# Optimization experiments

Hardware: AMD Instinct MI355X
Metric: run time of the kernel (lower is better)

Reference implementation:

```python
import jax, jax.numpy as jnp
import numpy as np

HEADS = 8
DIM_HEAD = 64
DOWN = 2

def setup_inputs() -> dict:
    key = jax.random.key(0)
    ks = jax.random.split(key, 6)
    shp = (1, 128, 16, 32, 32)
    inner = HEADS * DIM_HEAD  # 512
    return {
        "x": jax.random.normal(ks[0], shp, dtype=jnp.float32),
        "context": jax.random.normal(ks[1], shp, dtype=jnp.float32),
        "Wq": jax.random.normal(ks[2], (inner, 128), dtype=jnp.float32) * 0.02,
        "Wk": jax.random.normal(ks[3], (inner, 128), dtype=jnp.float32) * 0.02,
        "Wv": jax.random.normal(ks[4], (inner, 128), dtype=jnp.float32) * 0.02,
        "Wo": jax.random.normal(ks[5], (128, inner), dtype=jnp.float32) * 0.02,
    }

def _avg_pool3d(c, f):
    b, ch, d, h, w = c.shape
    return c.reshape(b, ch, d // f, f, h // f, f, w // f, f).mean(axis=(3, 5, 7))

def reference(x, context, Wq, Wk, Wv, Wo):
    b, c, d1, h1, w1 = x.shape
    n = d1 * h1 * w1
    scale = DIM_HEAD ** -0.5
    xf = x.reshape(b, c, n)  # [b, c, N]
    # 1x1x1 conv == channel matmul
    q = jnp.einsum('oc,bcn->bon', Wq, xf).reshape(b, HEADS, DIM_HEAD, n)
    q = jnp.swapaxes(q, -2, -1)  # [b, h, N, dh]
    ctx = _avg_pool3d(context, DOWN)
    _, _, d2, h2, w2 = ctx.shape
    m = d2 * h2 * w2
    cf = ctx.reshape(b, c, m)
    k = jnp.einsum('oc,bcm->bom', Wk, cf).reshape(b, HEADS, DIM_HEAD, m)  # [b,h,dh,M]
    v = jnp.einsum('oc,bcm->bom', Wv, cf).reshape(b, HEADS, DIM_HEAD, m)
    v = jnp.swapaxes(v, -2, -1)  # [b, h, M, dh]
    scores = jnp.einsum('bhnd,bhdm->bhnm', q, k) * scale  # [b,h,N,M]
    attn = jax.nn.softmax(scores, axis=-1)
    out = jnp.einsum('bhnm,bhmd->bhnd', attn, v)  # [b,h,N,dh]
    out = jnp.swapaxes(out, -2, -1).reshape(b, HEADS * DIM_HEAD, n)  # [b,inner,N]
    y = jnp.einsum('oc,bcn->bon', Wo, out)
    return y.reshape(b, -1, d1, h1, w1)
```

## Files before the change

### kernel.cpp

```cpp
#include <hip/hip_runtime.h>

#define N_TOK 16384
#define M_TOK 2048
#define NHEADS 8
#define DH 64
#define CIN 128
#define INNER 512

typedef __attribute__((ext_vector_type(8))) short bf16x8;
typedef __attribute__((ext_vector_type(16))) float f32x16;
typedef __attribute__((ext_vector_type(4))) unsigned int u32x4;
typedef __attribute__((ext_vector_type(2))) unsigned int u32x2;

__device__ __forceinline__ unsigned short f2bf(float f) {
    unsigned u = __float_as_uint(f);
    u += 0x7fff + ((u >> 16) & 1);
    return (unsigned short)(u >> 16);
}

__device__ __forceinline__ unsigned cvtpk(float lo, float hi) {
    unsigned r;
    asm("v_cvt_pk_bf16_f32 %0, %1, %2" : "=v"(r) : "v"(lo), "v"(hi));
    return r;
}

__device__ __forceinline__ bf16x8 mk_bf16x8(unsigned a, unsigned b, unsigned c, unsigned d) {
    union { u32x4 w; bf16x8 h; } u;
    u.w = (u32x4){a, b, c, d};
    return u.h;
}

__device__ __forceinline__ void gload16(const void* g, void* l) {
    __builtin_amdgcn_global_load_lds(
        (const __attribute__((address_space(1))) unsigned int*)g,
        (__attribute__((address_space(3))) unsigned int*)l, 16, 0, 0);
}

__global__ __launch_bounds__(256) void prep_k(const float* __restrict__ Wq,
                                              const float* __restrict__ Wo,
                                              const float* __restrict__ cin,
                                              unsigned short* __restrict__ Wqb,
                                              unsigned short* __restrict__ Wob,
                                              float* __restrict__ cout) {
    if (blockIdx.x < 64) {
        int i = (blockIdx.x * 256 + threadIdx.x) * 8;
        const float* src; unsigned short* dst; float sc;
        if (i < 65536) { src = Wq + i; dst = Wqb + i; sc = 0.125f; }
        else           { src = Wo + (i - 65536); dst = Wob + (i - 65536); sc = 1.0f; }
        float4 a = *reinterpret_cast<const float4*>(src);
        float4 b = *reinterpret_cast<const float4*>(src + 4);
        unsigned short u[8] = { f2bf(a.x * sc), f2bf(a.y * sc), f2bf(a.z * sc), f2bf(a.w * sc),
                                f2bf(b.x * sc), f2bf(b.y * sc), f2bf(b.z * sc), f2bf(b.w * sc) };
        *reinterpret_cast<uint4*>(dst) = *reinterpret_cast<uint4*>(u);
    } else {
        int idx = (blockIdx.x - 64) * 256 + threadIdx.x;
        int c = idx >> 11, m = idx & 2047;
        int d2 = m >> 8, h2 = (m >> 4) & 15, w2 = m & 15;
        const float* b = cin + c * 16384 + d2 * 2048 + h2 * 64 + w2 * 2;
        float s = b[0] + b[1] + b[32] + b[33] + b[1024] + b[1025] + b[1056] + b[1057];
        cout[idx] = s * 0.125f;
    }
}

__global__ __launch_bounds__(256) void xT_k(const float* __restrict__ x,
                                            unsigned short* __restrict__ xb) {
    __shared__ unsigned short tile[64 * 132];
    const int t = threadIdx.x;
    const int n0 = blockIdx.x * 128;
    const int cb = blockIdx.y * 64;
#pragma unroll
    for (int cc2 = 0; cc2 < 2; ++cc2)
#pragma unroll
        for (int lp = 0; lp < 4; ++lp) {
            int id = lp * 256 + t;
            int row = id >> 5, ch = id & 31;
            float4 v = *reinterpret_cast<const float4*>(
                &x[(size_t)(cb + cc2 * 32 + row) * N_TOK + n0 + ch * 4]);
            unsigned short u[4] = { f2bf(v.x), f2bf(v.y), f2bf(v.z), f2bf(v.w) };
            *reinterpret_cast<uint2*>(&tile[(cc2 * 32 + row) * 132 + ch * 4]) =
                *reinterpret_cast<uint2*>(u);
        }
    __syncthreads();
#pragma unroll
    for (int lp = 0; lp < 4; ++lp) {
        int id = lp * 256 + t;
        int n = id >> 3, cg = id & 7;
        unsigned short u[8];
#pragma unroll
        for (int j = 0; j < 8; ++j) u[j] = tile[(cg * 8 + j) * 132 + n];
        *reinterpret_cast<uint4*>(&xb[(size_t)(n0 + n) * 128 + cb + cg * 8]) =
            *reinterpret_cast<uint4*>(u);
    }
}

__global__ __launch_bounds__(256) void kvproj_k(const float* __restrict__ ctx,
                                                const float* __restrict__ Wk,
                                                const float* __restrict__ Wv,
                                                unsigned short* __restrict__ Kb,
                                                unsigned short* __restrict__ Vb) {
    const int m0 = (blockIdx.x * 256 + threadIdx.x) * 2;
    const int o0 = blockIdx.y * 8;
    const float* W = blockIdx.z ? Wv : Wk;
    float acc[8][2];
#pragma unroll
    for (int j = 0; j < 8; ++j) { acc[j][0] = 0.f; acc[j][1] = 0.f; }
    for (int c4 = 0; c4 < CIN / 4; ++c4) {
        float xa[4][2];
#pragma unroll
        for (int cc = 0; cc < 4; ++cc)
            *reinterpret_cast<float2*>(xa[cc]) =
                *reinterpret_cast<const float2*>(&ctx[(size_t)(c4 * 4 + cc) * M_TOK + m0]);
#pragma unroll
        for (int j = 0; j < 8; ++j) {
            float4 wv = *reinterpret_cast<const float4*>(&W[(o0 + j) * CIN + c4 * 4]);
#pragma unroll
            for (int k = 0; k < 2; ++k) {
                acc[j][k] = fmaf(wv.x, xa[0][k], acc[j][k]);
                acc[j][k] = fmaf(wv.y, xa[1][k], acc[j][k]);
                acc[j][k] = fmaf(wv.z, xa[2][k], acc[j][k]);
                acc[j][k] = fmaf(wv.w, xa[3][k], acc[j][k]);
            }
        }
    }
    if (blockIdx.z) {
#pragma unroll
        for (int j = 0; j < 8; ++j) {
            unsigned w0 = (unsigned)f2bf(acc[j][0]) | ((unsigned)f2bf(acc[j][1]) << 16);
            *reinterpret_cast<unsigned*>(&Vb[(size_t)(o0 + j) * M_TOK + m0]) = w0;
        }
    } else {
        const int h = o0 >> 6, d0 = o0 & 63;
#pragma unroll
        for (int k = 0; k < 2; ++k) {
            unsigned short u[8];
#pragma unroll
            for (int j = 0; j < 8; ++j) u[j] = f2bf(acc[j][k]);
            *reinterpret_cast<uint4*>(&Kb[((size_t)h * M_TOK + m0 + k) * DH + d0]) =
                *reinterpret_cast<uint4*>(u);
        }
    }
}

__global__ __launch_bounds__(256) void qproj_k(const unsigned short* __restrict__ Wqb,
                                               const unsigned short* __restrict__ xb,
                                               unsigned short* __restrict__ Qb) {
    const int t = threadIdx.x;
    const int w = t >> 6, l = t & 63;
    const int la = l & 31, lg = l >> 5;
    const int n = blockIdx.x * 32 + la;

    bf16x8 bx[8];
#pragma unroll
    for (int ks = 0; ks < 8; ++ks)
        bx[ks] = *reinterpret_cast<const bf16x8*>(xb + (size_t)n * 128 + ks * 16 + lg * 8);

    f32x16 acc[4];
#pragma unroll
    for (int os = 0; os < 4; ++os) acc[os] = (f32x16){0,0,0,0,0,0,0,0,0,0,0,0,0,0,0,0};

#pragma unroll
    for (int os = 0; os < 4; ++os) {
        const int row = w * 128 + os * 32 + la;
#pragma unroll
        for (int ks = 0; ks < 8; ++ks) {
            bf16x8 aw = *reinterpret_cast<const bf16x8*>(Wqb + (size_t)row * 128 + ks * 16 + lg * 8);
            acc[os] = __builtin_amdgcn_mfma_f32_32x32x16_bf16(aw, bx[ks], acc[os], 0, 0, 0);
        }
    }
#pragma unroll
    for (int os = 0; os < 4; ++os) {
        const int h = w * 2 + (os >> 1);
        const int dbase = (os & 1) * 32 + 4 * lg;
#pragma unroll
        for (int rr = 0; rr < 4; ++rr) {
            unsigned p0 = cvtpk(acc[os][rr * 4 + 0], acc[os][rr * 4 + 1]);
            unsigned p1 = cvtpk(acc[os][rr * 4 + 2], acc[os][rr * 4 + 3]);
            uint2 pv = make_uint2(p0, p1);
            *reinterpret_cast<uint2*>(&Qb[((size_t)h * N_TOK + n) * DH + dbase + rr * 8]) = pv;
        }
    }
}

__global__ __launch_bounds__(256, 4) void attn_k(const unsigned short* __restrict__ Qb,
                                                 const unsigned short* __restrict__ Kb,
                                                 const unsigned short* __restrict__ Vb,
                                                 unsigned short* __restrict__ Ob) {
    __shared__ __align__(16) char smem[33792];
    __shared__ float rsinv[128];

    const int t = threadIdx.x;
    const int w = t >> 6, l = t & 63;
    const int la = l & 31, lg = l >> 5;
    const int bid = blockIdx.x;
    const int h = bid & 7;
    const int n0 = (bid >> 3) * 128;

    bf16x8 aq[4];
    {
        const unsigned short* qrow = Qb + ((size_t)h * N_TOK + n0 + w * 32 + la) * DH + lg * 8;
#pragma unroll
        for (int ks = 0; ks < 4; ++ks)
            aq[ks] = *reinterpret_cast<const bf16x8*>(qrow + ks * 16);
    }

    const int klane = (l >> 3) * 128 + (((l & 7) ^ (l >> 3)) << 4);
    const int vlane = (l >> 3) * 4096 + (((l & 7) ^ (l >> 3)) << 4);
    const char* gK = (const char*)Kb + (size_t)h * M_TOK * DH * 2 + w * 2048 + klane;
    const char* gV = (const char*)Vb + (size_t)h * DH * M_TOK * 2 + (size_t)w * 65536 + vlane;
    char* lKw = smem + w * 2048;

    auto stage = [&](int b, int tile) {
        char* lK = lKw + b * 16384;
        const char* sK = gK + (size_t)tile * 8192;
        const char* sV = gV + (size_t)tile * 128;
        gload16(sK, lK);
        gload16(sK + 1024, lK + 1024);
        gload16(sV, lK + 8192);
        gload16(sV + 32768, lK + 8192 + 1024);
    };

    f32x16 oacc0 = {0,0,0,0,0,0,0,0,0,0,0,0,0,0,0,0};
    f32x16 oacc1 = {0,0,0,0,0,0,0,0,0,0,0,0,0,0,0,0};
    float rs = 0.f;

    stage(0, 0);
    __syncthreads();

#pragma unroll 2
    for (int mt = 0; mt < M_TOK / 64; ++mt) {
        const int cb = (mt & 1) * 16384;
        if (mt < M_TOK / 64 - 1) stage((mt & 1) ^ 1, mt + 1);

#pragma unroll
        for (int ms = 0; ms < 2; ++ms) {
            f32x16 sacc = {0,0,0,0,0,0,0,0,0,0,0,0,0,0,0,0};
            __builtin_amdgcn_s_setprio(1);
#pragma unroll
            for (int ks = 0; ks < 4; ++ks) {
                const int row = ms * 32 + la;
                bf16x8 ak = *reinterpret_cast<const bf16x8*>(
                    smem + cb + row * 128 + ((32 * ks + 16 * lg) ^ ((row & 7) << 4)));
                sacc = __builtin_amdgcn_mfma_f32_32x32x16_bf16(ak, aq[ks], sacc, 0, 0, 0);
            }
            __builtin_amdgcn_s_setprio(0);
            float p[16];
#pragma unroll
            for (int r = 0; r < 16; ++r) { p[r] = __expf(sacc[r]); rs += p[r]; }
            u32x2 s0 = __builtin_amdgcn_permlane32_swap(cvtpk(p[0], p[1]),  cvtpk(p[4], p[5]),  false, false);
            u32x2 s1 = __builtin_amdgcn_permlane32_swap(cvtpk(p[2], p[3]),  cvtpk(p[6], p[7]),  false, false);
            u32x2 s2 = __builtin_amdgcn_permlane32_swap(cvtpk(p[8], p[9]),  cvtpk(p[12], p[13]), false, false);
            u32x2 s3 = __builtin_amdgcn_permlane32_swap(cvtpk(p[10], p[11]), cvtpk(p[14], p[15]), false, false);
            bf16x8 pa0 = mk_bf16x8(s0.x, s1.x, s0.y, s1.y);
            bf16x8 pa1 = mk_bf16x8(s2.x, s3.x, s2.y, s3.y);
            __builtin_amdgcn_s_setprio(1);
            {
                const int vrow = la, vs = (vrow & 7) << 4;
                bf16x8 bv0 = *reinterpret_cast<const bf16x8*>(
                    smem + cb + 8192 + vrow * 128 + ((64 * ms + 16 * lg) ^ vs));
                bf16x8 bv1 = *reinterpret_cast<const bf16x8*>(
                    smem + cb + 8192 + vrow * 128 + ((64 * ms + 32 + 16 * lg) ^ vs));
                oacc0 = __builtin_amdgcn_mfma_f32_32x32x16_bf16(pa0, bv0, oacc0, 0, 0, 0);
                oacc0 = __builtin_amdgcn_mfma_f32_32x32x16_bf16(pa1, bv1, oacc0, 0, 0, 0);
            }
            {
                const int vrow = 32 + la, vs = (vrow & 7) << 4;
                bf16x8 bv0 = *reinterpret_cast<const bf16x8*>(
                    smem + cb + 8192 + vrow * 128 + ((64 * ms + 16 * lg) ^ vs));
                bf16x8 bv1 = *reinterpret_cast<const bf16x8*>(
                    smem + cb + 8192 + vrow * 128 + ((64 * ms + 32 + 16 * lg) ^ vs));
                oacc1 = __builtin_amdgcn_mfma_f32_32x32x16_bf16(pa0, bv0, oacc1, 0, 0, 0);
                oacc1 = __builtin_amdgcn_mfma_f32_32x32x16_bf16(pa1, bv1, oacc1, 0, 0, 0);
            }
            __builtin_amdgcn_s_setprio(0);
        }
        __syncthreads();
    }

    rs += __shfl_xor(rs, 32);
    if (lg == 0) rsinv[w * 32 + la] = 1.0f / rs;

    __syncthreads();
    float* Ot = reinterpret_cast<float*>(smem);
#pragma unroll
    for (int dt = 0; dt < 2; ++dt)
#pragma unroll
        for (int r = 0; r < 16; r += 2) {
            int d = dt * 32 + la;
            int n = w * 32 + (r & 3) + 8 * (r >> 2) + 4 * lg;
            float2 v;
            v.x = dt ? oacc1[r] : oacc0[r];
            v.y = dt ? oacc1[r + 1] : oacc0[r + 1];
            *reinterpret_cast<float2*>(&Ot[d * 132 + n]) = v;
        }
    __syncthreads();
#pragma unroll
    for (int i = 0; i < 4; ++i) {
        int chunk = i * 256 + t;
        int n = chunk & 127, dg = chunk >> 7;
        float rv = rsinv[n];
        unsigned q[4];
#pragma unroll
        for (int jj = 0; jj < 4; ++jj) {
            float a = Ot[(dg * 8 + jj * 2) * 132 + n] * rv;
            float b = Ot[(dg * 8 + jj * 2 + 1) * 132 + n] * rv;
            q[jj] = cvtpk(a, b);
        }
        *reinterpret_cast<uint4*>(&Ob[(size_t)(n0 + n) * INNER + h * 64 + dg * 8]) =
            *reinterpret_cast<uint4*>(q);
    }
}

__global__ __launch_bounds__(256) void yproj_k(const unsigned short* __restrict__ Wob,
                                               const unsigned short* __restrict__ Ob,
                                               float* __restrict__ y) {
    const int t = threadIdx.x;
    const int w = t >> 6, l = t & 63;
    const int la = l & 31, lg = l >> 5;
    const int n = blockIdx.x * 32 + la;
    const int row = w * 32 + la;

    f32x16 acc = {0,0,0,0,0,0,0,0,0,0,0,0,0,0,0,0};
#pragma unroll 8
    for (int ks = 0; ks < 32; ++ks) {
        bf16x8 bo = *reinterpret_cast<const bf16x8*>(Ob + (size_t)n * INNER + ks * 16 + lg * 8);
        bf16x8 aw = *reinterpret_cast<const bf16x8*>(Wob + (size_t)row * INNER + ks * 16 + lg * 8);
        acc = __builtin_amdgcn_mfma_f32_32x32x16_bf16(aw, bo, acc, 0, 0, 0);
    }
#pragma unroll
    for (int rr = 0; rr < 4; ++rr)
#pragma unroll
        for (int q = 0; q < 4; ++q) {
            int o = w * 32 + 4 * lg + rr * 8 + q;
            y[(size_t)o * N_TOK + n] = acc[rr * 4 + q];
        }
}

extern "C" void kernel_launch(void* const* d_in, const int* in_sizes, int n_in,
                              void* d_out, int out_size, void* d_ws, size_t ws_size,
                              hipStream_t stream) {
    const float* x   = (const float*)d_in[0];
    const float* ctx = (const float*)d_in[1];
    const float* Wq  = (const float*)d_in[2];
    const float* Wk  = (const float*)d_in[3];
    const float* Wv  = (const float*)d_in[4];
    const float* Wo  = (const float*)d_in[5];
    float* y = (float*)d_out;

    char* W = (char*)d_ws;
    float* ctxp         = (float*)(W);
    unsigned short* Kb  = (unsigned short*)(W + 1u  * (1 << 20));
    unsigned short* Vb  = (unsigned short*)(W + 3u  * (1 << 20));
    unsigned short* xb  = (unsigned short*)(W + 5u  * (1 << 20));
    unsigned short* Wqb = (unsigned short*)(W + 9u  * (1 << 20));
    unsigned short* Wob = (unsigned short*)(W + 9u  * (1 << 20) + (256 << 10));
    unsigned short* Qb  = (unsigned short*)(W + 10u * (1 << 20));
    unsigned short* Ob  = (unsigned short*)(W + 26u * (1 << 20));

    prep_k<<<dim3(64 + (CIN * M_TOK) / 256), 256, 0, stream>>>(Wq, Wo, ctx, Wqb, Wob, ctxp);
    xT_k<<<dim3(N_TOK / 128, 2), 256, 0, stream>>>(x, xb);
    kvproj_k<<<dim3(M_TOK / 512, INNER / 8, 2), 256, 0, stream>>>(ctxp, Wk, Wv, Kb, Vb);
    qproj_k<<<dim3(N_TOK / 32), 256, 0, stream>>>(Wqb, xb, Qb);
    attn_k<<<dim3(N_TOK / 128 * NHEADS), 256, 0, stream>>>(Qb, Kb, Vb, Ob);
    yproj_k<<<dim3(N_TOK / 32), 256, 0, stream>>>(Wob, Ob, y);
}
```

Measured before the change: 145.3 us.

## Enlarge attention blocks to 512 threads sharing 128-token K/V tiles

Doubles the attention workgroup from 4 to 8 waves covering 256 query rows, so each K/V tile loaded into shared memory is reused by twice as many waves. The K/V tile per iteration grows from 64 to 128 context tokens, with a cooperative swizzled load across all threads and 64KB of double-buffered LDS. The output transpose epilogue is split into two passes to fit the existing staging layout. This lowers global K/V traffic and barrier count per unit of work, but the larger LDS footprint and block size may reduce occupancy, and the grid has half as many blocks.

```diff
diff --git a/kernel.cpp b/kernel.cpp
--- a/kernel.cpp
+++ b/kernel.cpp
@@ -181,19 +181,19 @@
     }
 }
 
-__global__ __launch_bounds__(256, 4) void attn_k(const unsigned short* __restrict__ Qb,
+__global__ __launch_bounds__(512, 4) void attn_k(const unsigned short* __restrict__ Qb,
                                                  const unsigned short* __restrict__ Kb,
                                                  const unsigned short* __restrict__ Vb,
                                                  unsigned short* __restrict__ Ob) {
-    __shared__ __align__(16) char smem[33792];
-    __shared__ float rsinv[128];
+    __shared__ __align__(16) char smem[65536];
+    __shared__ float rsinv[256];
 
     const int t = threadIdx.x;
     const int w = t >> 6, l = t & 63;
     const int la = l & 31, lg = l >> 5;
     const int bid = blockIdx.x;
     const int h = bid & 7;
-    const int n0 = (bid >> 3) * 128;
+    const int n0 = (bid >> 3) * 256;
 
     bf16x8 aq[4];
     {
@@ -203,20 +203,21 @@
             aq[ks] = *reinterpret_cast<const bf16x8*>(qrow + ks * 16);
     }
 
-    const int klane = (l >> 3) * 128 + (((l & 7) ^ (l >> 3)) << 4);
-    const int vlane = (l >> 3) * 4096 + (((l & 7) ^ (l >> 3)) << 4);
-    const char* gK = (const char*)Kb + (size_t)h * M_TOK * DH * 2 + w * 2048 + klane;
-    const char* gV = (const char*)Vb + (size_t)h * DH * M_TOK * 2 + (size_t)w * 65536 + vlane;
-    char* lKw = smem + w * 2048;
+    const char* gK = (const char*)Kb + (size_t)h * M_TOK * 128;
+    const char* gV = (const char*)Vb + (size_t)h * DH * 4096;
 
     auto stage = [&](int b, int tile) {
-        char* lK = lKw + b * 16384;
-        const char* sK = gK + (size_t)tile * 8192;
-        const char* sV = gV + (size_t)tile * 128;
-        gload16(sK, lK);
-        gload16(sK + 1024, lK + 1024);
-        gload16(sV, lK + 8192);
-        gload16(sV + 32768, lK + 8192 + 1024);
+        char* buf = smem + b * 32768;
+#pragma unroll
+        for (int i = 0; i < 2; ++i) {
+            int c = t + i * 512;
+            int row = c >> 3, o16 = (c & 7) << 4;
+            gload16(gK + (size_t)(tile * 128 + row) * 128 + (o16 ^ ((row & 7) << 4)),
+                    buf + c * 16);
+            int vrow = c >> 4, vo16 = (c & 15) << 4;
+            gload16(gV + (size_t)vrow * 4096 + tile * 256 + (vo16 ^ ((vrow & 7) << 4)),
+                    buf + 16384 + c * 16);
+        }
     };
 
     f32x16 oacc0 = {0,0,0,0,0,0,0,0,0,0,0,0,0,0,0,0};
@@ -227,12 +228,12 @@
     __syncthreads();
 
 #pragma unroll 2
-    for (int mt = 0; mt < M_TOK / 64; ++mt) {
-        const int cb = (mt & 1) * 16384;
-        if (mt < M_TOK / 64 - 1) stage((mt & 1) ^ 1, mt + 1);
-
-#pragma unroll
-        for (int ms = 0; ms < 2; ++ms) {
+    for (int mt = 0; mt < M_TOK / 128; ++mt) {
+        const int cb = (mt & 1) * 32768;
+        if (mt < M_TOK / 128 - 1) stage((mt & 1) ^ 1, mt + 1);
+
+#pragma unroll
+        for (int ms = 0; ms < 4; ++ms) {
             f32x16 sacc = {0,0,0,0,0,0,0,0,0,0,0,0,0,0,0,0};
             __builtin_amdgcn_s_setprio(1);
 #pragma unroll
@@ -255,19 +256,17 @@
             __builtin_amdgcn_s_setprio(1);
             {
                 const int vrow = la, vs = (vrow & 7) << 4;
-                bf16x8 bv0 = *reinterpret_cast<const bf16x8*>(
-                    smem + cb + 8192 + vrow * 128 + ((64 * ms + 16 * lg) ^ vs));
-                bf16x8 bv1 = *reinterpret_cast<const bf16x8*>(
-                    smem + cb + 8192 + vrow * 128 + ((64 * ms + 32 + 16 * lg) ^ vs));
+                const char* vb = smem + cb + 16384 + vrow * 256;
+                bf16x8 bv0 = *reinterpret_cast<const bf16x8*>(vb + ((64 * ms + 16 * lg) ^ vs));
+                bf16x8 bv1 = *reinterpret_cast<const bf16x8*>(vb + ((64 * ms + 32 + 16 * lg) ^ vs));
                 oacc0 = __builtin_amdgcn_mfma_f32_32x32x16_bf16(pa0, bv0, oacc0, 0, 0, 0);
                 oacc0 = __builtin_amdgcn_mfma_f32_32x32x16_bf16(pa1, bv1, oacc0, 0, 0, 0);
             }
             {
                 const int vrow = 32 + la, vs = (vrow & 7) << 4;
-                bf16x8 bv0 = *reinterpret_cast<const bf16x8*>(
-                    smem + cb + 8192 + vrow * 128 + ((64 * ms + 16 * lg) ^ vs));
-                bf16x8 bv1 = *reinterpret_cast<const bf16x8*>(
-                    smem + cb + 8192 + vrow * 128 + ((64 * ms + 32 + 16 * lg) ^ vs));
+                const char* vb = smem + cb + 16384 + vrow * 256;
+                bf16x8 bv0 = *reinterpret_cast<const bf16x8*>(vb + ((64 * ms + 16 * lg) ^ vs));
+                bf16x8 bv1 = *reinterpret_cast<const bf16x8*>(vb + ((64 * ms + 32 + 16 * lg) ^ vs));
                 oacc1 = __builtin_amdgcn_mfma_f32_32x32x16_bf16(pa0, bv0, oacc1, 0, 0, 0);
                 oacc1 = __builtin_amdgcn_mfma_f32_32x32x16_bf16(pa1, bv1, oacc1, 0, 0, 0);
             }
@@ -279,34 +278,40 @@
     rs += __shfl_xor(rs, 32);
     if (lg == 0) rsinv[w * 32 + la] = 1.0f / rs;
 
-    __syncthreads();
     float* Ot = reinterpret_cast<float*>(smem);
 #pragma unroll
-    for (int dt = 0; dt < 2; ++dt)
-#pragma unroll
-        for (int r = 0; r < 16; r += 2) {
-            int d = dt * 32 + la;
-            int n = w * 32 + (r & 3) + 8 * (r >> 2) + 4 * lg;
-            float2 v;
-            v.x = dt ? oacc1[r] : oacc0[r];
-            v.y = dt ? oacc1[r + 1] : oacc0[r + 1];
-            *reinterpret_cast<float2*>(&Ot[d * 132 + n]) = v;
-        }
-    __syncthreads();
-#pragma unroll
-    for (int i = 0; i < 4; ++i) {
-        int chunk = i * 256 + t;
-        int n = chunk & 127, dg = chunk >> 7;
-        float rv = rsinv[n];
-        unsigned q[4];
-#pragma unroll
-        for (int jj = 0; jj < 4; ++jj) {
-            float a = Ot[(dg * 8 + jj * 2) * 132 + n] * rv;
-            float b = Ot[(dg * 8 + jj * 2 + 1) * 132 + n] * rv;
-            q[jj] = cvtpk(a, b);
-        }
-        *reinterpret_cast<uint4*>(&Ob[(size_t)(n0 + n) * INNER + h * 64 + dg * 8]) =
-            *reinterpret_cast<uint4*>(q);
+    for (int pass = 0; pass < 2; ++pass) {
+        __syncthreads();
+        if ((w >> 2) == pass) {
+            const int wl = w & 3;
+#pragma unroll
+            for (int dt = 0; dt < 2; ++dt)
+#pragma unroll
+                for (int r = 0; r < 16; r += 2) {
+                    int d = dt * 32 + la;
+                    int n = wl * 32 + (r & 3) + 8 * (r >> 2) + 4 * lg;
+                    float2 v;
+                    v.x = dt ? oacc1[r] : oacc0[r];
+                    v.y = dt ? oacc1[r + 1] : oacc0[r + 1];
+                    *reinterpret_cast<float2*>(&Ot[d * 132 + n]) = v;
+                }
+        }
+        __syncthreads();
+#pragma unroll
+        for (int i = 0; i < 2; ++i) {
+            int id = i * 512 + t;
+            int n = id & 127, dg = id >> 7;
+            float rv = rsinv[pass * 128 + n];
+            unsigned q[4];
+#pragma unroll
+            for (int jj = 0; jj < 4; ++jj) {
+                float a = Ot[(dg * 8 + jj * 2) * 132 + n] * rv;
+                float b = Ot[(dg * 8 + jj * 2 + 1) * 132 + n] * rv;
+                q[jj] = cvtpk(a, b);
+            }
+            *reinterpret_cast<uint4*>(&Ob[(size_t)(n0 + pass * 128 + n) * INNER + h * 64 + dg * 8]) =
+                *reinterpret_cast<uint4*>(q);
+        }
     }
 }
 
@@ -360,6 +365,6 @@
     xT_k<<<dim3(N_TOK / 128, 2), 256, 0, stream>>>(x, xb);
     kvproj_k<<<dim3(M_TOK / 512, INNER / 8, 2), 256, 0, stream>>>(ctxp, Wk, Wv, Kb, Vb);
     qproj_k<<<dim3(N_TOK / 32), 256, 0, stream>>>(Wqb, xb, Qb);
-    attn_k<<<dim3(N_TOK / 128 * NHEADS), 256, 0, stream>>>(Qb, Kb, Vb, Ob);
+    attn_k<<<dim3(N_TOK / 256 * NHEADS), 512, 0, stream>>>(Qb, Kb, Vb, Ob);
     yproj_k<<<dim3(N_TOK / 32), 256, 0, stream>>>(Wob, Ob, y);
 }
```

Result: faster. 139.6 us (-3.9%).
